# Kernel optimization log

Hardware: AMD Instinct MI355X
Metric: run time of the kernel (lower is better)

Reference implementation:

```python
import jax, jax.numpy as jnp
import numpy as np

B, T, D, E = 4, 512, 128, 256

def setup_inputs() -> dict:
    key = jax.random.key(0)
    ks = jax.random.split(key, 9)
    s = lambda k, shape, fan: jax.random.normal(k, shape, jnp.float32) * (1.0 / np.sqrt(fan))
    return {
        "x": jax.random.normal(ks[0], (B, T, D), jnp.float32),
        "gate_w": s(ks[1], (D, E), D),
        "gate_b": jnp.zeros((E,), jnp.float32),
        "expert_w": s(ks[2], (E, D, D), D),
        "w1": s(ks[3], (D, D), D),
        "b1": jnp.zeros((D,), jnp.float32),
        "w2": s(ks[4], (D, D), D),
        "b2": jnp.zeros((D,), jnp.float32),
    }

def reference(x, gate_w, gate_b, expert_w, w1, b1, w2, b2):
    n_experts = expert_w.shape[0]
    # Router: softmax gate over all experts, then top-2 renormalized
    gate_scores = jax.nn.softmax(x @ gate_w + gate_b, axis=-1)        # [B,T,E]
    top_v, top_i = jax.lax.top_k(gate_scores, 2)                      # [B,T,2]
    top_w = top_v / (jnp.sum(top_v, axis=-1, keepdims=True) + 1e-6)
    # Dense all-expert projection (as in original module)
    expert_outputs = jnp.einsum('btd,edo->bteo', x, expert_w)         # [B,T,E,D]
    # Sparse top-2 mask in dense [B,T,E] form
    mask = jnp.sum(jax.nn.one_hot(top_i, n_experts, dtype=x.dtype) * top_w[..., None], axis=2)  # [B,T,E]
    weighted_avg = jnp.einsum('bteo,bte->bto', expert_outputs, mask)  # [B,T,D]
    g = weighted_avg @ w1 + b1
    weighted_avg = g * jax.nn.sigmoid(g) * (weighted_avg @ w2 + b2)   # [B,T,D]
    # Variance consensus over experts, weighted by top-2 mask
    diff_sq = jnp.square(expert_outputs - weighted_avg[:, :, None, :])  # [B,T,E,D]
    weighted_var = jnp.einsum('bteo,bte->bto', diff_sq, mask)           # [B,T,D]
    consensus = jnp.exp(-jnp.mean(weighted_var, axis=-1))               # [B,T]
    return weighted_avg, consensus
```

## Files before the change

kernel.cpp:

```cpp
#include <hip/hip_runtime.h>
#include <math.h>

constexpr int kD   = 128;
constexpr int kE   = 256;
constexpr int kTok = 2048;

__global__ __launch_bounds__(256) void k_gate(
    const float* __restrict__ x, const float* __restrict__ gate_w,
    const float* __restrict__ gate_b,
    float2* __restrict__ tokinfo, int* __restrict__ top2)
{
    const int b  = blockIdx.x;
    const int t  = threadIdx.x;
    const int wv = t >> 6, ln = t & 63;

    __shared__ float xsT[kD][4];
    __shared__ float partf[4][4];
    __shared__ int   parti[4][4];
    __shared__ int   pi0s[4];
    __shared__ float pv0s[4];

    {
        const float2 v = *(const float2*)(x + ((size_t)(b * 4 + wv)) * kD + ln * 2);
        xsT[ln * 2 + 0][wv] = v.x;
        xsT[ln * 2 + 1][wv] = v.y;
    }
    __syncthreads();

    float lg[4];
    {
        const float bias = gate_b[t];
        lg[0] = lg[1] = lg[2] = lg[3] = bias;
    }
    #pragma unroll 8
    for (int d = 0; d < kD; ++d) {
        const float w = gate_w[d * kE + t];
        const float4 xv = *(const float4*)&xsT[d][0];
        lg[0] = fmaf(xv.x, w, lg[0]);
        lg[1] = fmaf(xv.y, w, lg[1]);
        lg[2] = fmaf(xv.z, w, lg[2]);
        lg[3] = fmaf(xv.w, w, lg[3]);
    }

    float m[4];
    #pragma unroll
    for (int j = 0; j < 4; ++j) m[j] = lg[j];
    #pragma unroll
    for (int s = 1; s < 64; s <<= 1) {
        #pragma unroll
        for (int j = 0; j < 4; ++j) m[j] = fmaxf(m[j], __shfl_xor(m[j], s));
    }
    if (ln == 0) {
        #pragma unroll
        for (int j = 0; j < 4; ++j) partf[wv][j] = m[j];
    }
    __syncthreads();
    float mx[4];
    #pragma unroll
    for (int j = 0; j < 4; ++j)
        mx[j] = fmaxf(fmaxf(partf[0][j], partf[1][j]), fmaxf(partf[2][j], partf[3][j]));
    __syncthreads();

    float ex[4], sm[4];
    #pragma unroll
    for (int j = 0; j < 4; ++j) { ex[j] = __expf(lg[j] - mx[j]); sm[j] = ex[j]; }
    #pragma unroll
    for (int s = 1; s < 64; s <<= 1) {
        #pragma unroll
        for (int j = 0; j < 4; ++j) sm[j] += __shfl_xor(sm[j], s);
    }
    if (ln == 0) {
        #pragma unroll
        for (int j = 0; j < 4; ++j) partf[wv][j] = sm[j];
    }
    __syncthreads();
    float p[4];
    #pragma unroll
    for (int j = 0; j < 4; ++j) {
        const float tot = partf[0][j] + partf[1][j] + partf[2][j] + partf[3][j];
        p[j] = ex[j] / tot;
    }
    __syncthreads();

    float v[4]; int ix[4];
    #pragma unroll
    for (int j = 0; j < 4; ++j) { v[j] = p[j]; ix[j] = t; }
    #pragma unroll
    for (int s = 1; s < 64; s <<= 1) {
        #pragma unroll
        for (int j = 0; j < 4; ++j) {
            const float ov = __shfl_xor(v[j], s);
            const int   oi = __shfl_xor(ix[j], s);
            if (ov > v[j] || (ov == v[j] && oi < ix[j])) { v[j] = ov; ix[j] = oi; }
        }
    }
    if (ln == 0) {
        #pragma unroll
        for (int j = 0; j < 4; ++j) { partf[wv][j] = v[j]; parti[wv][j] = ix[j]; }
    }
    __syncthreads();
    if (t < 4) {
        const int j = t;
        float bv = partf[0][j]; int bi = parti[0][j];
        #pragma unroll
        for (int w = 1; w < 4; ++w) {
            const float ov = partf[w][j]; const int oi = parti[w][j];
            if (ov > bv || (ov == bv && oi < bi)) { bv = ov; bi = oi; }
        }
        pv0s[j] = bv; pi0s[j] = bi;
    }
    __syncthreads();

    #pragma unroll
    for (int j = 0; j < 4; ++j) {
        v[j] = (t == pi0s[j]) ? -INFINITY : p[j];
        ix[j] = t;
    }
    #pragma unroll
    for (int s = 1; s < 64; s <<= 1) {
        #pragma unroll
        for (int j = 0; j < 4; ++j) {
            const float ov = __shfl_xor(v[j], s);
            const int   oi = __shfl_xor(ix[j], s);
            if (ov > v[j] || (ov == v[j] && oi < ix[j])) { v[j] = ov; ix[j] = oi; }
        }
    }
    if (ln == 0) {
        #pragma unroll
        for (int j = 0; j < 4; ++j) { partf[wv][j] = v[j]; parti[wv][j] = ix[j]; }
    }
    __syncthreads();
    if (t < 4) {
        const int j = t;
        float bv = partf[0][j]; int bi = parti[0][j];
        #pragma unroll
        for (int w = 1; w < 4; ++w) {
            const float ov = partf[w][j]; const int oi = parti[w][j];
            if (ov > bv || (ov == bv && oi < bi)) { bv = ov; bi = oi; }
        }
        const int tok = b * 4 + j;
        const float v0 = pv0s[j], v1 = bv;
        const float den = v0 + v1 + 1e-6f;
        tokinfo[tok] = make_float2(v0 / den, v1 / den);
        top2[tok] = pi0s[j] | (bi << 8);
    }
}

__global__ __launch_bounds__(1024) void k_expert(
    const float* __restrict__ x, const float* __restrict__ expert_w,
    const int* __restrict__ top2, float* __restrict__ ybuf)
{
    const int e  = blockIdx.x >> 1;
    const int hf = blockIdx.x & 1;
    const int t  = threadIdx.x;

    __shared__ float W[kD][64];
    __shared__ float xs[16][kD];
    __shared__ int   llist[kTok];
    __shared__ int   lcount;

    if (t == 0) lcount = 0;
    __syncthreads();

    #pragma unroll
    for (int k = 0; k < 2; ++k) {
        const int i = k * 1024 + t;
        const int pk = top2[i];
        if ((pk & 255) == e)        llist[atomicAdd(&lcount, 1)] = i * 2;
        if (((pk >> 8) & 255) == e) llist[atomicAdd(&lcount, 1)] = i * 2 + 1;
    }

    {
        const float* Wg = expert_w + (size_t)e * kD * kD + hf * 64;
        #pragma unroll
        for (int k = 0; k < 2; ++k) {
            const int f  = k * 1024 + t;
            const int r  = f >> 4;
            const int c4 = (f & 15) * 4;
            *(float4*)&W[r][c4] = *(const float4*)&Wg[(size_t)r * kD + c4];
        }
    }
    __syncthreads();
    const int n = lcount;

    const int Wv = t >> 6, ln = t & 63;
    for (int base = 0; base < n; base += 16) {
        const int m = min(16, n - base);
        for (int i = t; i < m * kD; i += 1024) {
            const int row = i >> 7, d = i & 127;
            const int ev = llist[base + row];
            xs[row][d] = x[(size_t)(ev >> 1) * kD + d];
        }
        __syncthreads();

        const int idx = base + Wv;
        if (idx < n) {
            float acc = 0.f;
            #pragma unroll 8
            for (int d = 0; d < kD; ++d)
                acc = fmaf(xs[Wv][d], W[d][ln], acc);
            const int ev = llist[idx];
            ybuf[((size_t)(ev >> 1) * 2 + (ev & 1)) * kD + hf * 64 + ln] = acc;
        }
        __syncthreads();
    }
}

__global__ __launch_bounds__(256) void k_swiglu(
    const float* __restrict__ ybuf, const float2* __restrict__ tokinfo,
    const float* __restrict__ w1m, const float* __restrict__ b1,
    const float* __restrict__ w2m, const float* __restrict__ b2,
    float* __restrict__ out_avg, float* __restrict__ out_cons)
{
    const int b = blockIdx.x;
    const int t = threadIdx.x;
    const int tok0 = b * 4;

    __shared__ float  ys[4 * 2 * kD];
    __shared__ float  wvT[kD][4];
    __shared__ float  vv[4][kD];
    __shared__ float  os[4][kD];
    __shared__ float2 ti[4];

    *(float4*)&ys[t * 4] = *(const float4*)&ybuf[(size_t)tok0 * 2 * kD + t * 4];
    if (t < 4) ti[t] = tokinfo[tok0 + t];
    __syncthreads();

    #pragma unroll
    for (int k = 0; k < 2; ++k) {
        const int idx = t * 2 + k;
        const int j = idx >> 7, o = idx & 127;
        const float2 w = ti[j];
        wvT[o][j] = w.x * ys[(j * 2 + 0) * kD + o] + w.y * ys[(j * 2 + 1) * kD + o];
    }
    __syncthreads();

    const int h = t >> 7, o = t & 127;
    const float* Wm = h ? w2m : w1m;
    const float bias = h ? b2[o] : b1[o];
    float a0 = bias, a1 = bias, a2 = bias, a3 = bias;
    #pragma unroll 4
    for (int d = 0; d < kD; ++d) {
        const float w = Wm[d * kD + o];
        const float4 xv = *(const float4*)&wvT[d][0];
        a0 = fmaf(xv.x, w, a0);
        a1 = fmaf(xv.y, w, a1);
        a2 = fmaf(xv.z, w, a2);
        a3 = fmaf(xv.w, w, a3);
    }
    if (h) { vv[0][o] = a0; vv[1][o] = a1; vv[2][o] = a2; vv[3][o] = a3; }
    __syncthreads();
    if (!h) {
        float gg[4] = {a0, a1, a2, a3};
        #pragma unroll
        for (int j = 0; j < 4; ++j) {
            const float g = gg[j];
            const float r = g * (1.f / (1.f + __expf(-g))) * vv[j][o];
            os[j][o] = r;
            out_avg[(size_t)(tok0 + j) * kD + o] = r;
        }
    }
    __syncthreads();

    const int wv = t >> 6, ln = t & 63;
    const float2 w = ti[wv];
    float s = 0.f;
    #pragma unroll
    for (int k = 0; k < 2; ++k) {
        const int oo = ln * 2 + k;
        const float ot = os[wv][oo];
        const float d0 = ys[(wv * 2 + 0) * kD + oo] - ot;
        const float d1 = ys[(wv * 2 + 1) * kD + oo] - ot;
        s += w.x * d0 * d0 + w.y * d1 * d1;
    }
    #pragma unroll
    for (int sft = 1; sft < 64; sft <<= 1) s += __shfl_xor(s, sft);
    if (ln == 0) out_cons[tok0 + wv] = __expf(-s * (1.0f / (float)kD));
}

extern "C" void kernel_launch(void* const* d_in, const int* in_sizes, int n_in,
                              void* d_out, int out_size, void* d_ws, size_t ws_size,
                              hipStream_t stream) {
    const float*  x        = (const float*)d_in[0];
    const float*  gate_w   = (const float*)d_in[1];
    const float*  gate_b   = (const float*)d_in[2];
    const float*  expert_w = (const float*)d_in[3];
    const float*  w1m      = (const float*)d_in[4];
    const float*  b1       = (const float*)d_in[5];
    const float*  w2m      = (const float*)d_in[6];
    const float*  b2       = (const float*)d_in[7];

    float* out_avg  = (float*)d_out;
    float* out_cons = out_avg + (size_t)kTok * kD;

    char*   ws      = (char*)d_ws;
    float2* tokinfo = (float2*)ws;
    int*    top2    = (int*)(ws + 16384);
    float*  ybuf    = (float*)(ws + 32768);

    k_gate  <<<kTok / 4, 256,  0, stream>>>(x, gate_w, gate_b, tokinfo, top2);
    k_expert<<<kE * 2,   1024, 0, stream>>>(x, expert_w, top2, ybuf);
    k_swiglu<<<kTok / 4, 256,  0, stream>>>(ybuf, tokinfo, w1m, b1, w2m, b2, out_avg, out_cons);
}
```

Before: 39.54 us.

## Fuse SwiGLU and consensus tail into expert kernel via per-token completion counters

Result: slower. 133.0 us (+236.2%).

```diff
diff --git a/kernel.cpp b/kernel.cpp
--- a/kernel.cpp
+++ b/kernel.cpp
@@ -8,11 +8,14 @@
 __global__ __launch_bounds__(256) void k_gate(
     const float* __restrict__ x, const float* __restrict__ gate_w,
     const float* __restrict__ gate_b,
-    float2* __restrict__ tokinfo, int* __restrict__ top2)
+    float2* __restrict__ tokinfo, int* __restrict__ top2,
+    int* __restrict__ done)
 {
     const int b  = blockIdx.x;
     const int t  = threadIdx.x;
     const int wv = t >> 6, ln = t & 63;
+
+    if (t < 4) done[b * 4 + t] = 0;
 
     __shared__ float xsT[kD][4];
     __shared__ float partf[4][4];
@@ -146,9 +149,13 @@
     }
 }
 
-__global__ __launch_bounds__(1024) void k_expert(
+__global__ __launch_bounds__(1024) void k_expert_tail(
     const float* __restrict__ x, const float* __restrict__ expert_w,
-    const int* __restrict__ top2, float* __restrict__ ybuf)
+    const int* __restrict__ top2, const float2* __restrict__ tokinfo,
+    const float* __restrict__ w1m, const float* __restrict__ b1,
+    const float* __restrict__ w2m, const float* __restrict__ b2,
+    float* __restrict__ ybuf, int* __restrict__ done,
+    float* __restrict__ out_avg, float* __restrict__ out_cons)
 {
     const int e  = blockIdx.x >> 1;
     const int hf = blockIdx.x & 1;
@@ -158,8 +165,14 @@
     __shared__ float xs[16][kD];
     __shared__ int   llist[kTok];
     __shared__ int   lcount;
-
-    if (t == 0) lcount = 0;
+    __shared__ float  ysh[2][kD];
+    __shared__ float  wav[kD];
+    __shared__ float  part[2][4][kD];
+    __shared__ float  red[kD];
+    __shared__ int    nwin;
+    __shared__ float2 tish;
+
+    if (t == 0) { lcount = 0; nwin = 0; }
     __syncthreads();
 
     #pragma unroll
@@ -192,7 +205,6 @@
             xs[row][d] = x[(size_t)(ev >> 1) * kD + d];
         }
         __syncthreads();
-
         const int idx = base + Wv;
         if (idx < n) {
             float acc = 0.f;
@@ -200,82 +212,77 @@
             for (int d = 0; d < kD; ++d)
                 acc = fmaf(xs[Wv][d], W[d][ln], acc);
             const int ev = llist[idx];
-            ybuf[((size_t)(ev >> 1) * 2 + (ev & 1)) * kD + hf * 64 + ln] = acc;
-        }
-        __syncthreads();
-    }
-}
-
-__global__ __launch_bounds__(256) void k_swiglu(
-    const float* __restrict__ ybuf, const float2* __restrict__ tokinfo,
-    const float* __restrict__ w1m, const float* __restrict__ b1,
-    const float* __restrict__ w2m, const float* __restrict__ b2,
-    float* __restrict__ out_avg, float* __restrict__ out_cons)
-{
-    const int b = blockIdx.x;
-    const int t = threadIdx.x;
-    const int tok0 = b * 4;
-
-    __shared__ float  ys[4 * 2 * kD];
-    __shared__ float  wvT[kD][4];
-    __shared__ float  vv[4][kD];
-    __shared__ float  os[4][kD];
-    __shared__ float2 ti[4];
-
-    *(float4*)&ys[t * 4] = *(const float4*)&ybuf[(size_t)tok0 * 2 * kD + t * 4];
-    if (t < 4) ti[t] = tokinfo[tok0 + t];
-    __syncthreads();
-
-    #pragma unroll
-    for (int k = 0; k < 2; ++k) {
-        const int idx = t * 2 + k;
-        const int j = idx >> 7, o = idx & 127;
-        const float2 w = ti[j];
-        wvT[o][j] = w.x * ys[(j * 2 + 0) * kD + o] + w.y * ys[(j * 2 + 1) * kD + o];
-    }
-    __syncthreads();
-
-    const int h = t >> 7, o = t & 127;
-    const float* Wm = h ? w2m : w1m;
-    const float bias = h ? b2[o] : b1[o];
-    float a0 = bias, a1 = bias, a2 = bias, a3 = bias;
-    #pragma unroll 4
-    for (int d = 0; d < kD; ++d) {
-        const float w = Wm[d * kD + o];
-        const float4 xv = *(const float4*)&wvT[d][0];
-        a0 = fmaf(xv.x, w, a0);
-        a1 = fmaf(xv.y, w, a1);
-        a2 = fmaf(xv.z, w, a2);
-        a3 = fmaf(xv.w, w, a3);
-    }
-    if (h) { vv[0][o] = a0; vv[1][o] = a1; vv[2][o] = a2; vv[3][o] = a3; }
-    __syncthreads();
-    if (!h) {
-        float gg[4] = {a0, a1, a2, a3};
-        #pragma unroll
-        for (int j = 0; j < 4; ++j) {
-            const float g = gg[j];
-            const float r = g * (1.f / (1.f + __expf(-g))) * vv[j][o];
-            os[j][o] = r;
-            out_avg[(size_t)(tok0 + j) * kD + o] = r;
-        }
-    }
-    __syncthreads();
-
-    const int wv = t >> 6, ln = t & 63;
-    const float2 w = ti[wv];
-    float s = 0.f;
-    #pragma unroll
-    for (int k = 0; k < 2; ++k) {
-        const int oo = ln * 2 + k;
-        const float ot = os[wv][oo];
-        const float d0 = ys[(wv * 2 + 0) * kD + oo] - ot;
-        const float d1 = ys[(wv * 2 + 1) * kD + oo] - ot;
-        s += w.x * d0 * d0 + w.y * d1 * d1;
-    }
-    #pragma unroll
-    for (int sft = 1; sft < 64; sft <<= 1) s += __shfl_xor(s, sft);
-    if (ln == 0) out_cons[tok0 + wv] = __expf(-s * (1.0f / (float)kD));
+            __hip_atomic_store(
+                &ybuf[((size_t)(ev >> 1) * 2 + (ev & 1)) * kD + hf * 64 + ln],
+                acc, __ATOMIC_RELAXED, __HIP_MEMORY_SCOPE_AGENT);
+        }
+        __syncthreads();
+    }
+
+    int mytok0 = -1, mytok1 = -1;
+    if (t < n)        mytok0 = llist[t] >> 1;
+    if (1024 + t < n) mytok1 = llist[1024 + t] >> 1;
+    __syncthreads();
+
+    if (mytok0 >= 0) {
+        const int old = __hip_atomic_fetch_add(&done[mytok0], 1,
+                          __ATOMIC_RELAXED, __HIP_MEMORY_SCOPE_AGENT);
+        if (old == 3) llist[atomicAdd(&nwin, 1)] = mytok0;
+    }
+    if (mytok1 >= 0) {
+        const int old = __hip_atomic_fetch_add(&done[mytok1], 1,
+                          __ATOMIC_RELAXED, __HIP_MEMORY_SCOPE_AGENT);
+        if (old == 3) llist[atomicAdd(&nwin, 1)] = mytok1;
+    }
+    __syncthreads();
+    const int wn = nwin;
+
+    for (int wi = 0; wi < wn; ++wi) {
+        const int tok = llist[wi];
+        if (t < 256) {
+            const float yv = __hip_atomic_load(&ybuf[(size_t)tok * 2 * kD + t],
+                               __ATOMIC_RELAXED, __HIP_MEMORY_SCOPE_AGENT);
+            ysh[t >> 7][t & 127] = yv;
+        }
+        if (t == 0) tish = tokinfo[tok];
+        __syncthreads();
+        if (t < kD) wav[t] = tish.x * ysh[0][t] + tish.y * ysh[1][t];
+        __syncthreads();
+        {
+            const int h = t >> 9, rem = t & 511, q = rem >> 7, o = rem & 127;
+            const float* Wm = h ? w2m : w1m;
+            const int d0 = q * 32;
+            float acc = 0.f;
+            #pragma unroll 8
+            for (int dd = 0; dd < 32; ++dd)
+                acc = fmaf(wav[d0 + dd], Wm[(size_t)(d0 + dd) * kD + o], acc);
+            part[h][q][o] = acc;
+        }
+        __syncthreads();
+        if (t < 256) {
+            const int h = t >> 7, o = t & 127;
+            const float s = part[h][0][o] + part[h][1][o] + part[h][2][o] + part[h][3][o]
+                            + (h ? b2[o] : b1[o]);
+            part[h][0][o] = s;
+        }
+        __syncthreads();
+        if (t < kD) {
+            const float g   = part[0][0][t];
+            const float vvv = part[1][0][t];
+            const float r = g * (1.f / (1.f + __expf(-g))) * vvv;
+            out_avg[(size_t)tok * kD + t] = r;
+            const float dd0 = ysh[0][t] - r, dd1 = ysh[1][t] - r;
+            red[t] = tish.x * dd0 * dd0 + tish.y * dd1 * dd1;
+        }
+        __syncthreads();
+        if (t < 64) {
+            float s = red[t] + red[t + 64];
+            #pragma unroll
+            for (int sft = 1; sft < 64; sft <<= 1) s += __shfl_xor(s, sft);
+            if (t == 0) out_cons[tok] = __expf(-s * (1.0f / (float)kD));
+        }
+        __syncthreads();
+    }
 }
 
 extern "C" void kernel_launch(void* const* d_in, const int* in_sizes, int n_in,
@@ -296,9 +303,11 @@
     char*   ws      = (char*)d_ws;
     float2* tokinfo = (float2*)ws;
     int*    top2    = (int*)(ws + 16384);
+    int*    done    = (int*)(ws + 24576);
     float*  ybuf    = (float*)(ws + 32768);
 
-    k_gate  <<<kTok / 4, 256,  0, stream>>>(x, gate_w, gate_b, tokinfo, top2);
-    k_expert<<<kE * 2,   1024, 0, stream>>>(x, expert_w, top2, ybuf);
-    k_swiglu<<<kTok / 4, 256,  0, stream>>>(ybuf, tokinfo, w1m, b1, w2m, b2, out_avg, out_cons);
+    k_gate<<<kTok / 4, 256, 0, stream>>>(x, gate_w, gate_b, tokinfo, top2, done);
+    k_expert_tail<<<kE * 2, 1024, 0, stream>>>(x, expert_w, top2, tokinfo,
+                                               w1m, b1, w2m, b2,
+                                               ybuf, done, out_avg, out_cons);
 }
```
